# Kernel tuning notes

Measured on AMD Instinct MI355X. Metric: run time of the kernel, lower is better.

Reference implementation:

```python
import jax, jax.numpy as jnp
import numpy as np

N = 20000
E = 320000
H = 16
C = 16
NUM_GRAPHS = 64
NEG_SLOPE = 0.2


def _gat(x, edge_index, W, a_src, a_dst, bias):
    # PyG GATConv, concat=True, shared lin for src/dst, eval mode (no dropout)
    h = (x @ W).reshape(-1, H, C)                       # [N,H,C]
    src, dst = edge_index[0], edge_index[1]
    alpha_src = jnp.sum(h * a_src, axis=-1)             # [N,H]
    alpha_dst = jnp.sum(h * a_dst, axis=-1)             # [N,H]
    alpha = alpha_src[src] + alpha_dst[dst]             # [E,H]
    alpha = jax.nn.leaky_relu(alpha, NEG_SLOPE)
    amax = jax.ops.segment_max(alpha, dst, num_segments=N)
    ex = jnp.exp(alpha - amax[dst])
    denom = jax.ops.segment_sum(ex, dst, num_segments=N)
    attn = ex / jnp.where(denom == 0, 1.0, denom)[dst]  # [E,H]
    msg = h[src] * attn[:, :, None]                     # [E,H,C]
    out = jax.ops.segment_sum(msg, dst, num_segments=N) # [N,H,C]
    return out.reshape(-1, H * C) + bias


def setup_inputs() -> dict:
    key = jax.random.key(0)
    ks = jax.random.split(key, 32)
    d = {}
    d['x'] = jax.random.normal(ks[0], (N, 20), dtype=jnp.float32)
    d['edge_index_ipv6'] = jax.random.randint(ks[1], (2, E), 0, N)
    d['edge_attr_ipv6'] = jax.random.normal(ks[2], (E, 19), dtype=jnp.float32)
    d['edge_index_tsch'] = jax.random.randint(ks[3], (2, E), 0, N)
    d['edge_attr_tsch'] = jax.random.normal(ks[4], (E, 7), dtype=jnp.float32)
    d['batch'] = jnp.sort(jax.random.randint(ks[5], (N,), 0, NUM_GRAPHS))
    s = 0.1
    d['W_i'] = jax.random.normal(ks[6], (20, H * C), dtype=jnp.float32) * s
    d['a_src_i'] = jax.random.normal(ks[7], (H, C), dtype=jnp.float32) * s
    d['a_dst_i'] = jax.random.normal(ks[8], (H, C), dtype=jnp.float32) * s
    d['b_i'] = jnp.zeros((H * C,), dtype=jnp.float32)
    d['W_t'] = jax.random.normal(ks[9], (20, H * C), dtype=jnp.float32) * s
    d['a_src_t'] = jax.random.normal(ks[10], (H, C), dtype=jnp.float32) * s
    d['a_dst_t'] = jax.random.normal(ks[11], (H, C), dtype=jnp.float32) * s
    d['b_t'] = jnp.zeros((H * C,), dtype=jnp.float32)
    d['Wf'] = jax.random.normal(ks[12], (512, 64), dtype=jnp.float32) * s
    d['bf'] = jnp.zeros((64,), dtype=jnp.float32)
    d['W1'] = jax.random.normal(ks[13], (64, 32), dtype=jnp.float32) * s
    d['b1'] = jnp.zeros((32,), dtype=jnp.float32)
    d['W2'] = jax.random.normal(ks[14], (32, 16), dtype=jnp.float32) * s
    d['b2'] = jnp.zeros((16,), dtype=jnp.float32)
    d['W3'] = jax.random.normal(ks[15], (16, 16), dtype=jnp.float32) * s
    d['b3'] = jnp.zeros((16,), dtype=jnp.float32)
    d['Wce'] = jax.random.normal(ks[16], (16, 3), dtype=jnp.float32) * s
    d['bce'] = jnp.zeros((3,), dtype=jnp.float32)
    d['Wcv'] = jax.random.normal(ks[17], (16, 3), dtype=jnp.float32) * s
    d['bcv'] = jnp.zeros((3,), dtype=jnp.float32)
    return d


def reference(x, edge_index_ipv6, edge_attr_ipv6, edge_index_tsch, edge_attr_tsch,
              batch, W_i, a_src_i, a_dst_i, b_i, W_t, a_src_t, a_dst_t, b_t,
              Wf, bf, W1, b1, W2, b2, W3, b3, Wce, bce, Wcv, bcv):
    # edge_attr_* are ignored by GATConv (edge_dim=None in PyG), as in original
    n_ipv6 = _gat(x, edge_index_ipv6, W_i, a_src_i, a_dst_i, b_i)
    n_tsch = _gat(x, edge_index_tsch, W_t, a_src_t, a_dst_t, b_t)
    h = jnp.concatenate([n_ipv6, n_tsch], axis=-1)      # [N,512]
    h = jax.nn.relu(h @ Wf + bf)
    h = jax.nn.relu(h @ W1 + b1)
    h = jax.nn.relu(h @ W2 + b2)
    h = jax.nn.relu(h @ W3 + b3)                        # [N,16]
    ssum = jax.ops.segment_sum(h, batch, num_segments=NUM_GRAPHS)
    cnt = jax.ops.segment_sum(jnp.ones((h.shape[0], 1), h.dtype), batch,
                              num_segments=NUM_GRAPHS)
    g = ssum / jnp.where(cnt == 0, 1.0, cnt)            # [G,16]
    out_event = g @ Wce + bce
    out_env = g @ Wcv + bcv
    return out_event, out_env
```

## Files before the change

kernel.cpp:

```cpp
#include <hip/hip_runtime.h>
#include <math.h>

#define N_NODES 20000
#define N_EDGES 320000
#define NG 64
#define NEG 0.2f
#define NCHUNK ((N_NODES + 255) / 256)

typedef __attribute__((ext_vector_type(8))) short bf16x8;
typedef __attribute__((ext_vector_type(4))) float f32x4;

__device__ __forceinline__ unsigned short f2bf(float f) {
  unsigned int u = __float_as_uint(f);
  return (unsigned short)((u + 0x7fffu + ((u >> 16) & 1u)) >> 16);
}

__global__ __launch_bounds__(256) void k_prep(
    const float* __restrict__ W_i, const float* __restrict__ as_i, const float* __restrict__ ad_i,
    const float* __restrict__ W_t, const float* __restrict__ as_t, const float* __restrict__ ad_t,
    const float* __restrict__ Wf, const float* __restrict__ bf,
    const float* __restrict__ b_i, const float* __restrict__ b_t,
    float* __restrict__ wsall, unsigned short* __restrict__ wbigfrag,
    float* __restrict__ bfold,
    int* __restrict__ fill_i, int* __restrict__ fill_t,
    float* __restrict__ gsum, int* __restrict__ gcnt) {
  __shared__ float bred[4][64];
  int idx = blockIdx.x * 256 + threadIdx.x;
  if (idx < 1280) {
    int k = idx >> 6, c = idx & 63;
    int set = c >> 5, role = (c >> 4) & 1, h = c & 15;
    const float* W = set ? W_t : W_i;
    const float* a = set ? (role ? ad_t : as_t) : (role ? ad_i : as_i);
    float v = 0.f;
#pragma unroll
    for (int j = 0; j < 16; ++j) v = fmaf(W[k * 256 + h * 16 + j], a[h * 16 + j], v);
    wsall[idx] = v;
    return;
  }
  idx -= 1280;
  if (idx < 49152) {
    int ct = idx / 12288, rem = idx % 12288;
    int lane = (rem >> 3) & 63, j = rem & 7, ks = rem >> 9;
    int k = ks * 32 + ((lane >> 4) << 3) + j;
    int nc = ct * 16 + (lane & 15);
    float v = 0.f;
    int g = (k >= 384) ? 1 : 0;
    int r = k - g * 384;
    int h = r / 24, c = r - h * 24;
    if (c < 20) {
      const float* W = g ? W_t : W_i;
      const float* wr = W + c * 256 + (h << 4);
      const float* wf = Wf + ((g << 8) + (h << 4)) * 64 + nc;
#pragma unroll
      for (int m = 0; m < 16; ++m) v = fmaf(wr[m], wf[m * 64], v);
    }
    wbigfrag[idx] = f2bf(v);
    return;
  }
  idx -= 49152;
  if (idx < 256) {
    int t = threadIdx.x, wv = t >> 6, j = t & 63;
    float p = 0.f;
    int i0 = wv * 128;
#pragma unroll 4
    for (int i = i0; i < i0 + 128; ++i) {
      float b = (i < 256) ? b_i[i] : b_t[i - 256];
      p = fmaf(b, Wf[i * 64 + j], p);
    }
    bred[wv][j] = p;
    __syncthreads();
    if (wv == 0) bfold[j] = bred[0][j] + bred[1][j] + bred[2][j] + bred[3][j] + bf[j];
    return;
  }
  idx -= 256;
  if (idx < N_NODES) { fill_i[idx] = 0; return; }
  idx -= N_NODES;
  if (idx < N_NODES) { fill_t[idx] = 0; return; }
  idx -= N_NODES;
  if (idx < NG * 16) { gsum[idx] = 0.f; return; }
  idx -= NG * 16;
  if (idx < NG) gcnt[idx] = 0;
}

__global__ __launch_bounds__(256) void k_alpha(
    const float* __restrict__ x, const float* __restrict__ wsall,
    float* __restrict__ xpad,
    float* __restrict__ asrc0, float* __restrict__ adst0,
    float* __restrict__ asrc1, float* __restrict__ adst1) {
  int t = threadIdx.x;
  int n0 = blockIdx.x * 16;
  __shared__ float xs[16][20];
  __shared__ float ws[20][64];
  for (int i = t; i < 16 * 20; i += 256) {
    int nd = i / 20, k = i % 20;
    xs[nd][k] = x[(n0 + nd) * 20 + k];
  }
  for (int i = t; i < 1280; i += 256) ws[i >> 6][i & 63] = wsall[i];
  __syncthreads();
  for (int i = t; i < 512; i += 256) {
    int nd = i >> 5, j = i & 31;
    xpad[(size_t)(n0 + nd) * 32 + j] = (j < 20) ? xs[nd][j] : 0.f;
  }
#pragma unroll
  for (int i = 0; i < 4; ++i) {
    int wi = i * 256 + t;
    int nd = wi >> 6, c = wi & 63;
    float v = 0.f;
#pragma unroll
    for (int k = 0; k < 20; ++k) v = fmaf(xs[nd][k], ws[k][c], v);
    int n = n0 + nd, h = c & 15;
    float* arr = (c >> 5) ? ((c >> 4) & 1 ? adst1 : asrc1)
                          : ((c >> 4) & 1 ? adst0 : asrc0);
    arr[n * 16 + h] = v;
  }
}

__global__ void k_hist(const int* __restrict__ ei0, const int* __restrict__ ei1,
                       int* __restrict__ cnt0, int* __restrict__ cnt1) {
  int e = blockIdx.x * blockDim.x + threadIdx.x;
  if (e >= N_EDGES) return;
  if (blockIdx.y == 0)
    atomicAdd(&cnt0[ei0[N_EDGES + e]], 1);
  else
    atomicAdd(&cnt1[ei1[N_EDGES + e]], 1);
}

__global__ __launch_bounds__(256) void k_scan1(
    const int* __restrict__ cnt0, const int* __restrict__ cnt1,
    int* __restrict__ tmp0, int* __restrict__ tmp1, int* __restrict__ csums) {
  int chunk = blockIdx.x, set = blockIdx.y;
  const int* cnt = set ? cnt1 : cnt0;
  int* tmp = set ? tmp1 : tmp0;
  int t = threadIdx.x, lane = t & 63, wv = t >> 6;
  int i = chunk * 256 + t;
  int v = (i < N_NODES) ? cnt[i] : 0;
  int s = v;
#pragma unroll
  for (int d = 1; d < 64; d <<= 1) {
    int o = __shfl_up(s, d);
    if (lane >= d) s += o;
  }
  __shared__ int wsum[4];
  if (lane == 63) wsum[wv] = s;
  __syncthreads();
  int pre = 0;
#pragma unroll
  for (int j = 0; j < 4; ++j)
    if (j < wv) pre += wsum[j];
  s += pre;
  if (i < N_NODES) tmp[i] = s;
  if (t == 255) csums[set * 128 + chunk] = s;
}

__global__ __launch_bounds__(256) void k_scan3(
    const int* __restrict__ tmp0, const int* __restrict__ tmp1,
    const int* __restrict__ csums,
    int* __restrict__ rp0, int* __restrict__ rp1,
    int* __restrict__ fill0, int* __restrict__ fill1) {
  int chunk = blockIdx.x, set = blockIdx.y;
  const int* tmp = set ? tmp1 : tmp0;
  int* rp = set ? rp1 : rp0;
  int* fill = set ? fill1 : fill0;
  __shared__ int soff;
  if (threadIdx.x == 0) {
    int acc = 0;
    for (int cc = 0; cc < chunk; ++cc) acc += csums[set * 128 + cc];
    soff = acc;
  }
  __syncthreads();
  int off = soff;
  int i = chunk * 256 + threadIdx.x;
  if (i >= N_NODES) return;
  int incl = tmp[i];
  int c = fill[i];
  int excl = off + incl - c;
  rp[i] = excl;
  fill[i] = excl;
  if (i == N_NODES - 1) rp[N_NODES] = off + incl;
}

__global__ void k_scatter(const int* __restrict__ ei0, const int* __restrict__ ei1,
                          int* __restrict__ fill0, int* __restrict__ fill1,
                          unsigned short* __restrict__ srcs0,
                          unsigned short* __restrict__ srcs1) {
  int e = blockIdx.x * blockDim.x + threadIdx.x;
  if (e >= N_EDGES) return;
  const int* ei = blockIdx.y ? ei1 : ei0;
  int* fill = blockIdx.y ? fill1 : fill0;
  unsigned short* srcs = blockIdx.y ? srcs1 : srcs0;
  int d = ei[N_EDGES + e];
  int pos = atomicAdd(&fill[d], 1);
  srcs[pos] = (unsigned short)ei[e];
}

__global__ __launch_bounds__(256) void k_gat(
    const float* __restrict__ xpad,
    const float* __restrict__ asrc0, const float* __restrict__ adst0,
    const float* __restrict__ asrc1, const float* __restrict__ adst1,
    const int* __restrict__ rp0, const unsigned short* __restrict__ srcs0,
    const int* __restrict__ rp1, const unsigned short* __restrict__ srcs1,
    unsigned short* __restrict__ xagg) {
  __shared__ float xsh[4][16][36];
  __shared__ float lath[4][16][16];
  int w4 = threadIdx.x >> 6, lane = threadIdx.x & 63;
  int n = blockIdx.x * 2 + (w4 >> 1);
  int g = w4 & 1;
  int h16 = lane & 15, e4 = lane >> 4;
  int eid = lane & 15, slot = lane >> 4;
  float (*xs)[36] = xsh[w4];
  float (*la)[16] = lath[w4];
  const float* asrc = g ? asrc1 : asrc0;
  const float* adst = g ? adst1 : adst0;
  const int* rp = g ? rp1 : rp0;
  const unsigned short* srcs = g ? srcs1 : srcs0;
  int k0 = rp[n], k1 = rp[n + 1];
  float adn = adst[n * 16 + h16];
  float lacc = 0.f;
  float xa[8];
#pragma unroll
  for (int j = 0; j < 8; ++j) xa[j] = 0.f;
  if (k1 > k0) {
    int sb = (int)srcs[min(k0 + eid, k1 - 1)];
    for (int base = k0; base < k1; base += 16) {
      int sbN = 0;
      if (base + 16 < k1) sbN = (int)srcs[min(base + 16 + eid, k1 - 1)];
      float4 xv0 = *(const float4*)&xpad[(size_t)sb * 32 + slot * 8];
      float4 xv1 = *(const float4*)&xpad[(size_t)sb * 32 + slot * 8 + 4];
      float ex[4];
#pragma unroll
      for (int q = 0; q < 4; ++q) {
        int e = e4 + 4 * q;
        int s = __shfl(sb, e);
        float aa = asrc[s * 16 + h16] + adn;
        aa = aa >= 0.f ? aa : NEG * aa;
        ex[q] = (base + e < k1) ? __expf(aa) : 0.f;
        lacc += ex[q];
        la[e][h16] = ex[q];
      }
      *(float4*)&xs[eid][slot * 8] = xv0;
      *(float4*)&xs[eid][slot * 8 + 4] = xv1;
#pragma unroll
      for (int e = 0; e < 16; ++e) {
        float w = la[e][h16];
        float4 x0 = *(const float4*)&xs[e][e4 * 8];
        float4 x1 = *(const float4*)&xs[e][e4 * 8 + 4];
        xa[0] = fmaf(w, x0.x, xa[0]); xa[1] = fmaf(w, x0.y, xa[1]);
        xa[2] = fmaf(w, x0.z, xa[2]); xa[3] = fmaf(w, x0.w, xa[3]);
        xa[4] = fmaf(w, x1.x, xa[4]); xa[5] = fmaf(w, x1.y, xa[5]);
        xa[6] = fmaf(w, x1.z, xa[6]); xa[7] = fmaf(w, x1.w, xa[7]);
      }
      sb = sbN;
    }
  }
  float lh = lacc + __shfl_xor(lacc, 16);
  lh += __shfl_xor(lh, 32);
  float invl = lh > 0.f ? 1.f / lh : 0.f;
  if (e4 < 3) {
    unsigned int u[4];
#pragma unroll
    for (int q = 0; q < 4; ++q)
      u[q] = (unsigned int)f2bf(xa[2 * q] * invl) |
             ((unsigned int)f2bf(xa[2 * q + 1] * invl) << 16);
    *(uint4*)&xagg[(size_t)n * 768 + g * 384 + h16 * 24 + e4 * 8] = *(uint4*)u;
  }
}

__global__ __launch_bounds__(256) void k_mlp(
    const unsigned short* __restrict__ xagg, const unsigned short* __restrict__ wbigfrag,
    const float* __restrict__ bfold,
    const float* __restrict__ W1m, const float* __restrict__ b1v,
    const float* __restrict__ W2m, const float* __restrict__ b2v,
    const float* __restrict__ W3m, const float* __restrict__ b3v,
    const int* __restrict__ batch,
    float* __restrict__ gsum, int* __restrict__ gcnt) {
  int t = threadIdx.x, w = t >> 6, lane = t & 63;
  int n0 = blockIdx.x * 16;
  __shared__ float o1[16][68];
  __shared__ float o2[16][36];
  __shared__ float o3[16][20];
  __shared__ float o4[16][17];
  __shared__ int bs[16];
  if (t < 16) bs[t] = batch[n0 + t];

  {
    int m = lane & 15, kb = lane >> 4;
    const unsigned short* aptr = xagg + (size_t)(n0 + m) * 768 + kb * 8;
    const unsigned short* bbase = wbigfrag + (size_t)w * 12288 + lane * 8;
    f32x4 acc = {0.f, 0.f, 0.f, 0.f};
#pragma unroll 6
    for (int ks = 0; ks < 24; ++ks) {
      bf16x8 af = *(const bf16x8*)(aptr + ks * 32);
      bf16x8 bfr = *(const bf16x8*)(bbase + (size_t)ks * 512);
      acc = __builtin_amdgcn_mfma_f32_16x16x32_bf16(af, bfr, acc, 0, 0, 0);
    }
    int col = lane & 15, rg = lane >> 4;
#pragma unroll
    for (int r = 0; r < 4; ++r) {
      int row = rg * 4 + r;
      o1[row][w * 16 + col] = fmaxf(acc[r] + bfold[w * 16 + col], 0.f);
    }
  }
  __syncthreads();
  int nd = t >> 4, js = t & 15;
  {
    float a0 = b1v[js], a1 = b1v[js + 16];
#pragma unroll 8
    for (int k = 0; k < 64; ++k) {
      float hv = o1[nd][k];
      a0 = fmaf(hv, W1m[k * 32 + js], a0);
      a1 = fmaf(hv, W1m[k * 32 + js + 16], a1);
    }
    o2[nd][js] = fmaxf(a0, 0.f);
    o2[nd][js + 16] = fmaxf(a1, 0.f);
  }
  __syncthreads();
  {
    float a = b2v[js];
#pragma unroll
    for (int k = 0; k < 32; ++k) a = fmaf(o2[nd][k], W2m[k * 16 + js], a);
    o3[nd][js] = fmaxf(a, 0.f);
  }
  __syncthreads();
  {
    float a = b3v[js];
#pragma unroll
    for (int k = 0; k < 16; ++k) a = fmaf(o3[nd][k], W3m[k * 16 + js], a);
    o4[nd][js] = fmaxf(a, 0.f);
  }
  __syncthreads();
  if (t < 128) {
    int s = t >> 4, jx = t & 15;
    int b = bs[0] + s;
    if (b <= bs[15]) {
      float sum = 0.f; int c = 0;
#pragma unroll
      for (int ndd = 0; ndd < 16; ++ndd)
        if (bs[ndd] == b) { sum += o4[ndd][jx]; ++c; }
      if (c > 0) {
        atomicAdd(&gsum[b * 16 + jx], sum);
        if (jx == 0) atomicAdd(&gcnt[b], c);
      }
    }
  }
}

__global__ void k_head(const float* __restrict__ gsum, const int* __restrict__ gcnt,
                       const float* __restrict__ Wce, const float* __restrict__ bce,
                       const float* __restrict__ Wcv, const float* __restrict__ bcv,
                       float* __restrict__ out) {
  int t = threadIdx.x;
  if (t >= 384) return;
  int half = t / 192, idx = t % 192;
  int b = idx / 3, r = idx % 3;
  float cnt = (float)gcnt[b];
  float inv = cnt > 0.f ? 1.f / cnt : 1.f;
  const float* Wc = half ? Wcv : Wce;
  const float* bc = half ? bcv : bce;
  float v = bc[r];
#pragma unroll
  for (int j = 0; j < 16; ++j) v = fmaf(gsum[b * 16 + j] * inv, Wc[j * 3 + r], v);
  out[t] = v;
}

extern "C" void kernel_launch(void* const* d_in, const int* in_sizes, int n_in,
                              void* d_out, int out_size, void* d_ws, size_t ws_size,
                              hipStream_t stream) {
  const float* x = (const float*)d_in[0];
  const int* ei_i = (const int*)d_in[1];
  const int* ei_t = (const int*)d_in[3];
  const int* batch = (const int*)d_in[5];
  const float* W_i = (const float*)d_in[6];
  const float* as_i = (const float*)d_in[7];
  const float* ad_i = (const float*)d_in[8];
  const float* b_i = (const float*)d_in[9];
  const float* W_t = (const float*)d_in[10];
  const float* as_t = (const float*)d_in[11];
  const float* ad_t = (const float*)d_in[12];
  const float* b_t = (const float*)d_in[13];
  const float* Wf = (const float*)d_in[14];
  const float* bf = (const float*)d_in[15];
  const float* W1 = (const float*)d_in[16];
  const float* b1 = (const float*)d_in[17];
  const float* W2 = (const float*)d_in[18];
  const float* b2 = (const float*)d_in[19];
  const float* W3 = (const float*)d_in[20];
  const float* b3 = (const float*)d_in[21];
  const float* Wce = (const float*)d_in[22];
  const float* bce = (const float*)d_in[23];
  const float* Wcv = (const float*)d_in[24];
  const float* bcv = (const float*)d_in[25];

  char* ws = (char*)d_ws;
  size_t off = 0;
  auto take = [&](size_t bytes) {
    void* p = ws + off;
    off = (off + bytes + 255) & ~(size_t)255;
    return p;
  };
  float* xpad = (float*)take((size_t)N_NODES * 32 * 4);
  unsigned short* xagg = (unsigned short*)take((size_t)N_NODES * 768 * 2);
  float* wsall = (float*)take((size_t)1280 * 4);
  unsigned short* wbigfrag = (unsigned short*)take((size_t)49152 * 2);
  float* bfold = (float*)take((size_t)64 * 4);
  float* asrc_i = (float*)take((size_t)N_NODES * 16 * 4);
  float* adst_i = (float*)take((size_t)N_NODES * 16 * 4);
  float* asrc_t = (float*)take((size_t)N_NODES * 16 * 4);
  float* adst_t = (float*)take((size_t)N_NODES * 16 * 4);
  int* rowptr_i = (int*)take((size_t)(N_NODES + 1) * 4);
  int* rowptr_t = (int*)take((size_t)(N_NODES + 1) * 4);
  int* fill_i = (int*)take((size_t)N_NODES * 4);
  int* fill_t = (int*)take((size_t)N_NODES * 4);
  int* tmp_i = (int*)take((size_t)N_NODES * 4);
  int* tmp_t = (int*)take((size_t)N_NODES * 4);
  int* csums = (int*)take((size_t)2 * 128 * 4);
  unsigned short* srcs_i = (unsigned short*)take((size_t)N_EDGES * 2);
  unsigned short* srcs_t = (unsigned short*)take((size_t)N_EDGES * 2);
  float* gsum = (float*)take((size_t)NG * 16 * 4);
  int* gcnt = (int*)take((size_t)NG * 4);

  int prep_items = 1280 + 49152 + 256 + N_NODES + N_NODES + NG * 16 + NG;
  k_prep<<<(prep_items + 255) / 256, 256, 0, stream>>>(
      W_i, as_i, ad_i, W_t, as_t, ad_t, Wf, bf, b_i, b_t,
      wsall, wbigfrag, bfold, fill_i, fill_t, gsum, gcnt);

  k_alpha<<<N_NODES / 16, 256, 0, stream>>>(x, wsall, xpad,
                                            asrc_i, adst_i, asrc_t, adst_t);

  dim3 egrid((N_EDGES + 255) / 256, 2);
  k_hist<<<egrid, 256, 0, stream>>>(ei_i, ei_t, fill_i, fill_t);
  dim3 sgrid(NCHUNK, 2);
  k_scan1<<<sgrid, 256, 0, stream>>>(fill_i, fill_t, tmp_i, tmp_t, csums);
  k_scan3<<<sgrid, 256, 0, stream>>>(tmp_i, tmp_t, csums, rowptr_i, rowptr_t,
                                     fill_i, fill_t);
  k_scatter<<<egrid, 256, 0, stream>>>(ei_i, ei_t, fill_i, fill_t, srcs_i, srcs_t);

  k_gat<<<N_NODES / 2, 256, 0, stream>>>(xpad, asrc_i, adst_i, asrc_t, adst_t,
                                         rowptr_i, srcs_i, rowptr_t, srcs_t,
                                         xagg);

  k_mlp<<<N_NODES / 16, 256, 0, stream>>>(xagg, wbigfrag, bfold,
                                          W1, b1, W2, b2, W3, b3,
                                          batch, gsum, gcnt);

  k_head<<<1, 384, 0, stream>>>(gsum, gcnt, Wce, bce, Wcv, bcv, (float*)d_out);
}
```

Baseline: 163.1 us.

## Merge scan passes via flag-based chunk aggregates; prefetch GAT gathers one batch ahead

```diff
diff --git a/kernel.cpp b/kernel.cpp
--- a/kernel.cpp
+++ b/kernel.cpp
@@ -6,6 +6,7 @@
 #define NG 64
 #define NEG 0.2f
 #define NCHUNK ((N_NODES + 255) / 256)
+#define FLAGBIT (1 << 30)
 
 typedef __attribute__((ext_vector_type(8))) short bf16x8;
 typedef __attribute__((ext_vector_type(4))) float f32x4;
@@ -23,7 +24,7 @@
     float* __restrict__ wsall, unsigned short* __restrict__ wbigfrag,
     float* __restrict__ bfold,
     int* __restrict__ fill_i, int* __restrict__ fill_t,
-    float* __restrict__ gsum, int* __restrict__ gcnt) {
+    float* __restrict__ gsum, int* __restrict__ gcnt, int* __restrict__ aggs) {
   __shared__ float bred[4][64];
   int idx = blockIdx.x * 256 + threadIdx.x;
   if (idx < 1280) {
@@ -79,7 +80,9 @@
   idx -= N_NODES;
   if (idx < NG * 16) { gsum[idx] = 0.f; return; }
   idx -= NG * 16;
-  if (idx < NG) gcnt[idx] = 0;
+  if (idx < NG) { gcnt[idx] = 0; return; }
+  idx -= NG;
+  if (idx < 256) aggs[idx] = 0;
 }
 
 __global__ __launch_bounds__(256) void k_alpha(
@@ -125,15 +128,16 @@
     atomicAdd(&cnt1[ei1[N_EDGES + e]], 1);
 }
 
-__global__ __launch_bounds__(256) void k_scan1(
-    const int* __restrict__ cnt0, const int* __restrict__ cnt1,
-    int* __restrict__ tmp0, int* __restrict__ tmp1, int* __restrict__ csums) {
+__global__ __launch_bounds__(256) void k_scan(
+    int* __restrict__ fill0, int* __restrict__ fill1,
+    int* __restrict__ rp0, int* __restrict__ rp1,
+    int* __restrict__ aggs) {
   int chunk = blockIdx.x, set = blockIdx.y;
-  const int* cnt = set ? cnt1 : cnt0;
-  int* tmp = set ? tmp1 : tmp0;
+  int* fill = set ? fill1 : fill0;
+  int* rp = set ? rp1 : rp0;
   int t = threadIdx.x, lane = t & 63, wv = t >> 6;
   int i = chunk * 256 + t;
-  int v = (i < N_NODES) ? cnt[i] : 0;
+  int v = (i < N_NODES) ? fill[i] : 0;
   int s = v;
 #pragma unroll
   for (int d = 1; d < 64; d <<= 1) {
@@ -148,35 +152,33 @@
   for (int j = 0; j < 4; ++j)
     if (j < wv) pre += wsum[j];
   s += pre;
-  if (i < N_NODES) tmp[i] = s;
-  if (t == 255) csums[set * 128 + chunk] = s;
-}
-
-__global__ __launch_bounds__(256) void k_scan3(
-    const int* __restrict__ tmp0, const int* __restrict__ tmp1,
-    const int* __restrict__ csums,
-    int* __restrict__ rp0, int* __restrict__ rp1,
-    int* __restrict__ fill0, int* __restrict__ fill1) {
-  int chunk = blockIdx.x, set = blockIdx.y;
-  const int* tmp = set ? tmp1 : tmp0;
-  int* rp = set ? rp1 : rp0;
-  int* fill = set ? fill1 : fill0;
-  __shared__ int soff;
-  if (threadIdx.x == 0) {
-    int acc = 0;
-    for (int cc = 0; cc < chunk; ++cc) acc += csums[set * 128 + cc];
-    soff = acc;
-  }
-  __syncthreads();
-  int off = soff;
-  int i = chunk * 256 + threadIdx.x;
-  if (i >= N_NODES) return;
-  int incl = tmp[i];
-  int c = fill[i];
-  int excl = off + incl - c;
-  rp[i] = excl;
-  fill[i] = excl;
-  if (i == N_NODES - 1) rp[N_NODES] = off + incl;
+  int agg = wsum[0] + wsum[1] + wsum[2] + wsum[3];
+  if (t == 0)
+    __hip_atomic_store(&aggs[set * 128 + chunk], agg | FLAGBIT,
+                       __ATOMIC_RELEASE, __HIP_MEMORY_SCOPE_AGENT);
+  __shared__ int reds[256];
+  int part = 0;
+  for (int j = t; j < chunk; j += 256) {
+    int a;
+    do {
+      a = __hip_atomic_load(&aggs[set * 128 + j], __ATOMIC_ACQUIRE,
+                            __HIP_MEMORY_SCOPE_AGENT);
+    } while (!(a & FLAGBIT));
+    part += a & (FLAGBIT - 1);
+  }
+  reds[t] = part;
+  __syncthreads();
+  for (int st = 128; st > 0; st >>= 1) {
+    if (t < st) reds[t] += reds[t + st];
+    __syncthreads();
+  }
+  int carry = reds[0];
+  int excl = carry + s - v;
+  if (i < N_NODES) {
+    rp[i] = excl;
+    fill[i] = excl;
+    if (i == N_NODES - 1) rp[N_NODES] = excl + v;
+  }
 }
 
 __global__ void k_scatter(const int* __restrict__ ei0, const int* __restrict__ ei1,
@@ -214,34 +216,45 @@
   const int* rp = g ? rp1 : rp0;
   const unsigned short* srcs = g ? srcs1 : srcs0;
   int k0 = rp[n], k1 = rp[n + 1];
-  float adn = adst[n * 16 + h16];
+  float4 adn4 = *(const float4*)&adst[n * 16 + slot * 4];
   float lacc = 0.f;
   float xa[8];
 #pragma unroll
   for (int j = 0; j < 8; ++j) xa[j] = 0.f;
   if (k1 > k0) {
+    int nbat = (k1 - k0 + 15) >> 4;
     int sb = (int)srcs[min(k0 + eid, k1 - 1)];
-    for (int base = k0; base < k1; base += 16) {
-      int sbN = 0;
-      if (base + 16 < k1) sbN = (int)srcs[min(base + 16 + eid, k1 - 1)];
-      float4 xv0 = *(const float4*)&xpad[(size_t)sb * 32 + slot * 8];
-      float4 xv1 = *(const float4*)&xpad[(size_t)sb * 32 + slot * 8 + 4];
-      float ex[4];
-#pragma unroll
-      for (int q = 0; q < 4; ++q) {
-        int e = e4 + 4 * q;
-        int s = __shfl(sb, e);
-        float aa = asrc[s * 16 + h16] + adn;
-        aa = aa >= 0.f ? aa : NEG * aa;
-        ex[q] = (base + e < k1) ? __expf(aa) : 0.f;
-        lacc += ex[q];
-        la[e][h16] = ex[q];
+    float4 xv0 = *(const float4*)&xpad[(size_t)sb * 32 + slot * 8];
+    float4 xv1 = *(const float4*)&xpad[(size_t)sb * 32 + slot * 8 + 4];
+    float4 av4 = *(const float4*)&asrc[(size_t)sb * 16 + slot * 4];
+    int sbN = 0;
+    if (nbat > 1) sbN = (int)srcs[min(k0 + 16 + eid, k1 - 1)];
+    for (int bb = 0; bb < nbat; ++bb) {
+      float4 xv0N = {0.f,0.f,0.f,0.f}, xv1N = xv0N, av4N = xv0N;
+      int sbNN = 0;
+      if (bb + 1 < nbat) {
+        xv0N = *(const float4*)&xpad[(size_t)sbN * 32 + slot * 8];
+        xv1N = *(const float4*)&xpad[(size_t)sbN * 32 + slot * 8 + 4];
+        av4N = *(const float4*)&asrc[(size_t)sbN * 16 + slot * 4];
+      }
+      if (bb + 2 < nbat)
+        sbNN = (int)srcs[min(k0 + (bb + 2) * 16 + eid, k1 - 1)];
+      bool val = (k0 + bb * 16 + eid) < k1;
+      float4 ex4;
+      {
+        float a;
+        a = av4.x + adn4.x; a = a >= 0.f ? a : NEG * a; ex4.x = val ? __expf(a) : 0.f;
+        a = av4.y + adn4.y; a = a >= 0.f ? a : NEG * a; ex4.y = val ? __expf(a) : 0.f;
+        a = av4.z + adn4.z; a = a >= 0.f ? a : NEG * a; ex4.z = val ? __expf(a) : 0.f;
+        a = av4.w + adn4.w; a = a >= 0.f ? a : NEG * a; ex4.w = val ? __expf(a) : 0.f;
       }
       *(float4*)&xs[eid][slot * 8] = xv0;
       *(float4*)&xs[eid][slot * 8 + 4] = xv1;
+      *(float4*)&la[eid][slot * 4] = ex4;
 #pragma unroll
       for (int e = 0; e < 16; ++e) {
         float w = la[e][h16];
+        lacc += w;
         float4 x0 = *(const float4*)&xs[e][e4 * 8];
         float4 x1 = *(const float4*)&xs[e][e4 * 8 + 4];
         xa[0] = fmaf(w, x0.x, xa[0]); xa[1] = fmaf(w, x0.y, xa[1]);
@@ -249,12 +262,10 @@
         xa[4] = fmaf(w, x1.x, xa[4]); xa[5] = fmaf(w, x1.y, xa[5]);
         xa[6] = fmaf(w, x1.z, xa[6]); xa[7] = fmaf(w, x1.w, xa[7]);
       }
-      sb = sbN;
-    }
-  }
-  float lh = lacc + __shfl_xor(lacc, 16);
-  lh += __shfl_xor(lh, 32);
-  float invl = lh > 0.f ? 1.f / lh : 0.f;
+      xv0 = xv0N; xv1 = xv1N; av4 = av4N; sb = sbN; sbN = sbNN;
+    }
+  }
+  float invl = lacc > 0.f ? 1.f / lacc : 0.f;
   if (e4 < 3) {
     unsigned int u[4];
 #pragma unroll
@@ -410,18 +421,16 @@
   int* rowptr_t = (int*)take((size_t)(N_NODES + 1) * 4);
   int* fill_i = (int*)take((size_t)N_NODES * 4);
   int* fill_t = (int*)take((size_t)N_NODES * 4);
-  int* tmp_i = (int*)take((size_t)N_NODES * 4);
-  int* tmp_t = (int*)take((size_t)N_NODES * 4);
   int* csums = (int*)take((size_t)2 * 128 * 4);
   unsigned short* srcs_i = (unsigned short*)take((size_t)N_EDGES * 2);
   unsigned short* srcs_t = (unsigned short*)take((size_t)N_EDGES * 2);
   float* gsum = (float*)take((size_t)NG * 16 * 4);
   int* gcnt = (int*)take((size_t)NG * 4);
 
-  int prep_items = 1280 + 49152 + 256 + N_NODES + N_NODES + NG * 16 + NG;
+  int prep_items = 1280 + 49152 + 256 + N_NODES + N_NODES + NG * 16 + NG + 256;
   k_prep<<<(prep_items + 255) / 256, 256, 0, stream>>>(
       W_i, as_i, ad_i, W_t, as_t, ad_t, Wf, bf, b_i, b_t,
-      wsall, wbigfrag, bfold, fill_i, fill_t, gsum, gcnt);
+      wsall, wbigfrag, bfold, fill_i, fill_t, gsum, gcnt, csums);
 
   k_alpha<<<N_NODES / 16, 256, 0, stream>>>(x, wsall, xpad,
                                             asrc_i, adst_i, asrc_t, adst_t);
@@ -429,9 +438,7 @@
   dim3 egrid((N_EDGES + 255) / 256, 2);
   k_hist<<<egrid, 256, 0, stream>>>(ei_i, ei_t, fill_i, fill_t);
   dim3 sgrid(NCHUNK, 2);
-  k_scan1<<<sgrid, 256, 0, stream>>>(fill_i, fill_t, tmp_i, tmp_t, csums);
-  k_scan3<<<sgrid, 256, 0, stream>>>(tmp_i, tmp_t, csums, rowptr_i, rowptr_t,
-                                     fill_i, fill_t);
+  k_scan<<<sgrid, 256, 0, stream>>>(fill_i, fill_t, rowptr_i, rowptr_t, csums);
   k_scatter<<<egrid, 256, 0, stream>>>(ei_i, ei_t, fill_i, fill_t, srcs_i, srcs_t);
 
   k_gat<<<N_NODES / 2, 256, 0, stream>>>(xpad, asrc_i, adst_i, asrc_t, adst_t,
```

Result: no change. 165.1 us (+1.2%).
